# Performance work log

Hardware: AMD Instinct MI355X
Metric: run time of the kernel (lower is better)

The kernel has to match this reference:

```python
import jax, jax.numpy as jnp
import numpy as np

B, CIN, COUT, H, W = 8, 64, 64, 96, 96
K = 3
PAD = 1
BN_EPS = 1e-5


def conv2d(x, w, b):
    # plain 3x3 conv, stride 1, pad 1 (NCHW / OIHW)
    y = jax.lax.conv_general_dilated(
        x, w, window_strides=(1, 1), padding=[(PAD, PAD), (PAD, PAD)],
        dimension_numbers=("NCHW", "OIHW", "NCHW"))
    return y + b[None, :, None, None]


def setup_inputs() -> dict:
    key = jax.random.key(0)
    ks = jax.random.split(key, 6)
    s = 0.05  # small init so offsets stay near the regular grid (matches DCN zero-ish init)
    return {
        "x": jax.random.normal(ks[0], (B, CIN, H, W), jnp.float32),
        "offset_w": jax.random.normal(ks[1], (2 * K * K, CIN, K, K), jnp.float32) * s,
        "offset_b": jnp.zeros((2 * K * K,), jnp.float32),
        "mod_w": jax.random.normal(ks[2], (K * K, CIN, K, K), jnp.float32) * s,
        "mod_b": jnp.zeros((K * K,), jnp.float32),
        "weight": jax.random.normal(ks[3], (COUT, CIN, K, K), jnp.float32) * s,
        "bias": jax.random.normal(ks[4], (COUT,), jnp.float32) * s,
        "bn_gamma": jnp.ones((COUT,), jnp.float32),
        "bn_beta": jnp.zeros((COUT,), jnp.float32),
        "bn_mean": jnp.zeros((COUT,), jnp.float32),
        "bn_var": jnp.ones((COUT,), jnp.float32),
    }


def _deform_sample(xb, py, px):
    # xb: [C,H,W]; py, px: [K2,H,W] fractional sampling coords (zero outside image)
    y0 = jnp.floor(py)
    x0 = jnp.floor(px)
    dy = py - y0
    dx = px - x0

    def gather(yi, xi):
        valid = ((yi >= 0) & (yi < H) & (xi >= 0) & (xi < W)).astype(xb.dtype)
        yc = jnp.clip(yi, 0, H - 1).astype(jnp.int32)
        xc = jnp.clip(xi, 0, W - 1).astype(jnp.int32)
        return xb[:, yc, xc] * valid  # [C,K2,H,W]

    v00 = gather(y0, x0)
    v01 = gather(y0, x0 + 1.0)
    v10 = gather(y0 + 1.0, x0)
    v11 = gather(y0 + 1.0, x0 + 1.0)
    return (v00 * (1 - dy) * (1 - dx) + v01 * (1 - dy) * dx
            + v10 * dy * (1 - dx) + v11 * dy * dx)  # [C,K2,H,W]


def reference(x, offset_w, offset_b, mod_w, mod_b, weight, bias,
              bn_gamma, bn_beta, bn_mean, bn_var):
    # 1) predict offsets and modulation mask (DCNv2)
    offset = conv2d(x, offset_w, offset_b)                 # [B, 2*K2, H, W]
    modulator = 2.0 * jax.nn.sigmoid(conv2d(x, mod_w, mod_b))  # [B, K2, H, W]

    off = offset.reshape(B, K * K, 2, H, W)
    off_y, off_x = off[:, :, 0], off[:, :, 1]              # [B,K2,H,W]

    # 2) base sampling grid per kernel tap
    ky, kx = jnp.meshgrid(jnp.arange(K), jnp.arange(K), indexing="ij")
    base_y = (jnp.arange(H)[None, :, None] - PAD
              + ky.reshape(-1)[:, None, None]).astype(jnp.float32)  # [K2,H,1]
    base_x = (jnp.arange(W)[None, None, :] - PAD
              + kx.reshape(-1)[:, None, None]).astype(jnp.float32)  # [K2,1,W]
    py = base_y + off_y                                    # [B,K2,H,W]
    px = base_x + off_x

    # 3) bilinear gather at irregular positions, modulate per tap
    sampled = jax.vmap(_deform_sample)(x, py, px)          # [B,C,K2,H,W]
    sampled = sampled * modulator[:, None]                 # broadcast over C

    # 4) contract taps with the regular conv weight
    wk = weight.reshape(COUT, CIN, K * K)
    y = jnp.einsum("bckhw,ock->bohw", sampled, wk) + bias[None, :, None, None]

    # 5) BatchNorm (inference: running stats) + ReLU
    inv = bn_gamma / jnp.sqrt(bn_var + BN_EPS)
    y = (y - bn_mean[None, :, None, None]) * inv[None, :, None, None] \
        + bn_beta[None, :, None, None]
    return jax.nn.relu(y)
```

## Files before the change

kernel.cpp:

```cpp
#include <hip/hip_runtime.h>
#include <hip/hip_bf16.h>
#include <hip/hip_fp16.h>
#include <math.h>

#define BB 8
#define HH 96
#define WW 96
#define HW 9216
#define BN_EPS 1e-5f

typedef _Float16 f16x8 __attribute__((ext_vector_type(8)));
typedef float f32x4 __attribute__((ext_vector_type(4)));

union HU { _Float16 h; unsigned short u; };

#define OFF_W4   0
#define SZ_W4    (BB*9*HW*16)
#define OFF_XT   (OFF_W4 + SZ_W4)
#define SZ_XT    (BB*HW*64*2)
#define OFF_XY   (OFF_XT + SZ_XT)
#define SZ_XY    (BB*9*HW*4)
#define OFF_WB   (OFF_XY + SZ_XY)
#define SZ_WB    (64*576*2)
#define OFF_WO   (OFF_WB + SZ_WB)
#define SZ_WO    (32*576*2)
#define OFF_BN   (OFF_WO + SZ_WO)
#define SZ_BN    (64*2*4)

__global__ __launch_bounds__(256) void prep_kernel(
    const float* __restrict__ weight, const float* __restrict__ offw,
    const float* __restrict__ modw,
    const float* __restrict__ bias, const float* __restrict__ gamma,
    const float* __restrict__ beta, const float* __restrict__ mean,
    const float* __restrict__ var,
    _Float16* __restrict__ wB, _Float16* __restrict__ wOff,
    float* __restrict__ bnS, float* __restrict__ bnB) {
  int tid = blockIdx.x * 256 + threadIdx.x;
  if (tid < 64 * 576) {
    int o = tid / 576, ck = tid % 576;
    int k = ck >> 6, c = ck & 63;
    wB[tid] = (_Float16)weight[o * 576 + c * 9 + k];
  }
  int t2 = tid - 64 * 576;
  if (t2 >= 0 && t2 < 32 * 576) {
    int oc = t2 / 576, kcol = t2 % 576;
    int kk = kcol >> 6, c = kcol & 63;
    float v = 0.f;
    if (oc < 18)      v = offw[(oc * 64 + c) * 9 + kk];
    else if (oc < 27) v = modw[((oc - 18) * 64 + c) * 9 + kk];
    wOff[t2] = (_Float16)v;
  }
  int t3 = tid - (64 * 576 + 32 * 576);
  if (t3 >= 0 && t3 < 64) {
    float inv = gamma[t3] * rsqrtf(var[t3] + BN_EPS);
    bnS[t3] = inv;
    bnB[t3] = (bias[t3] - mean[t3]) * inv + beta[t3];
  }
}

__global__ __launch_bounds__(256) void transpose_x_kernel(
    const float* __restrict__ x, _Float16* __restrict__ xT) {
  __shared__ float tile[64][65];
  int tid = threadIdx.x;
  int b = blockIdx.x & 7;
  int hwb = (blockIdx.x >> 3) * 64;
  int col = tid & 63, g = tid >> 6;
  float r[16];
#pragma unroll
  for (int it = 0; it < 16; ++it)
    r[it] = x[(b * 64 + it * 4 + g) * HW + hwb + col];
  __builtin_amdgcn_sched_barrier(0);
#pragma unroll
  for (int it = 0; it < 16; ++it)
    tile[it * 4 + g][col] = r[it];
  __syncthreads();
#pragma unroll
  for (int it = 0; it < 16; ++it) {
    int p = it * 4 + g;
    xT[(size_t)(b * HW + hwb + p) * 64 + col] = (_Float16)tile[col][p];
  }
}

__global__ __launch_bounds__(256, 8) void conv_offsets_kernel(
    const _Float16* __restrict__ xTh, const _Float16* __restrict__ wOff,
    const float* __restrict__ offb, const float* __restrict__ modb,
    float4* __restrict__ w4, unsigned* __restrict__ xy) {
  __shared__ __attribute__((aligned(16))) _Float16 sN[3 * 34 * 70];
  __shared__ float o_off[32 * 33];

  int tid = threadIdx.x;
  int lane = tid & 63;
  int wv = __builtin_amdgcn_readfirstlane(tid >> 6);

  int bi = blockIdx.x;
  int b = bi & 7, rem = bi >> 3;
  int h = rem / 3, w0 = (rem % 3) * 32;

  const _Float16* xb = xTh + (size_t)b * HW * 64;
  _Float16 sv[26];
#pragma unroll
  for (int i = 0; i < 26; ++i) {
    int p = wv + 4 * i;
    _Float16 v = (_Float16)0.f;
    if (p < 102) {
      int row = p / 34, col = p - row * 34;
      int y = h + row - 1, xx = w0 + col - 1;
      if ((y >= 0) && (y < HH) && (xx >= 0) && (xx < WW))
        v = xb[(size_t)(y * WW + xx) * 64 + lane];
    }
    sv[i] = v;
  }
  __builtin_amdgcn_sched_barrier(0);
#pragma unroll
  for (int i = 0; i < 26; ++i) {
    int p = wv + 4 * i;
    if (p < 102) {
      int row = p / 34, col = p - row * 34;
      sN[(row * 34 + col) * 70 + lane] = sv[i];
    }
  }
  __syncthreads();

  int r = lane & 15, g = lane >> 4;
  int mt = wv >> 1, nt = wv & 1;
  int px = mt * 16 + r;
  const _Float16* bp = wOff + (nt * 16 + r) * 576 + g * 8;
  f32x4 acc = {0.f, 0.f, 0.f, 0.f};
#pragma unroll
  for (int s = 0; s < 18; ++s) {
    int kk = s >> 1, ky = kk / 3, kx = kk - ky * 3;
    f16x8 a = *(const f16x8*)&sN[(ky * 34 + px + kx) * 70 + (s & 1) * 32 + g * 8];
    f16x8 bb = *(const f16x8*)(bp + s * 32);
    acc = __builtin_amdgcn_mfma_f32_16x16x32_f16(a, bb, acc, 0, 0, 0);
  }
#pragma unroll
  for (int j = 0; j < 4; ++j)
    o_off[(mt * 16 + g * 4 + j) * 33 + nt * 16 + r] = acc[j];
  __syncthreads();

  for (int it = tid; it < 288; it += 256) {
    int pxx = it & 31, k = it >> 5;
    int ky = k / 3, kx = k - ky * 3;
    int w = w0 + pxx;

    float offy = o_off[pxx * 33 + 2 * k]     + offb[2 * k];
    float offx = o_off[pxx * 33 + 2 * k + 1] + offb[2 * k + 1];
    float mod  = 2.f / (1.f + __expf(-(o_off[pxx * 33 + 18 + k] + modb[k])));

    float py  = (float)(h - 1 + ky) + offy;
    float px_ = (float)(w - 1 + kx) + offx;
    float y0f = floorf(py), x0f = floorf(px_);
    float dy = py - y0f, dx = px_ - x0f;
    int y0 = (int)y0f, x0 = (int)x0f;
    int y1 = y0 + 1, x1 = x0 + 1;
    bool vy0 = (y0 >= 0) && (y0 < HH), vy1 = (y1 >= 0) && (y1 < HH);
    bool vx0 = (x0 >= 0) && (x0 < WW), vx1 = (x1 >= 0) && (x1 < WW);
    float w00 = (vy0 && vx0) ? (1.f - dy) * (1.f - dx) * mod : 0.f;
    float w01 = (vy0 && vx1) ? (1.f - dy) * dx * mod : 0.f;
    float w10 = (vy1 && vx0) ? dy * (1.f - dx) * mod : 0.f;
    float w11 = (vy1 && vx1) ? dy * dx * mod : 0.f;
    int y0c = min(max(y0, 0), HH - 1), y1c = min(max(y1, 0), HH - 1);
    int x0c = min(max(x0, 0), WW - 1), x1c = min(max(x1, 0), WW - 1);
    unsigned pk = (unsigned)y0c | ((unsigned)y1c << 8) |
                  ((unsigned)x0c << 16) | ((unsigned)x1c << 24);
    int idx = (b * 9 + k) * HW + h * WW + w;
    w4[idx] = make_float4(w00, w01, w10, w11);
    xy[idx] = pk;
  }
}

__device__ __forceinline__ float hf(unsigned u) {
  HU h; h.u = (unsigned short)u; return (float)h.h;
}

__global__ __launch_bounds__(256, 4) void dcn_main_kernel(
    const _Float16* __restrict__ xT,
    const float4* __restrict__ w4, const unsigned* __restrict__ xy,
    const _Float16* __restrict__ wB,
    const float* __restrict__ bnS, const float* __restrict__ bnB,
    float* __restrict__ out) {
  __shared__ __attribute__((aligned(16))) _Float16 s_A[16 * 584];
  float* o_lds = (float*)s_A;

  int tid = threadIdx.x;
  int lane = tid & 63;
  int wv = __builtin_amdgcn_readfirstlane(tid >> 6);

  int bi = blockIdx.x;
  int b = bi & 7, t = bi >> 3;
  int h = t / 6, w0 = (t - (t / 6) * 6) * 16;
  int hwrow = h * WW + w0;

  const _Float16* xb = xT + (size_t)b * HW * 64;
  unsigned lane2 = (unsigned)(lane << 1);

  float4 wjA[9], wjB[9];
  unsigned rA[36], rB[36];

#define ISSUE(RES, WJ, P)                                                    \
  {                                                                          \
    int hw = hwrow + wv * 4 + (P);                                           \
    _Pragma("unroll")                                                        \
    for (int k = 0; k < 9; ++k) {                                            \
      int idx = (b * 9 + k) * HW + hw;                                       \
      unsigned q = xy[idx];                                                  \
      WJ[k] = w4[idx];                                                       \
      unsigned y0 = q & 255u, y1 = (q >> 8) & 255u;                          \
      unsigned x0 = (q >> 16) & 255u, x1 = q >> 24;                          \
      unsigned s00 = (y0 * WW + x0) << 7, s01 = (y0 * WW + x1) << 7;         \
      unsigned s10 = (y1 * WW + x0) << 7, s11 = (y1 * WW + x1) << 7;         \
      asm volatile("global_load_ushort %0, %1, %2"                           \
                   : "=v"(RES[4 * k + 0]) : "v"(s00 + lane2), "s"(xb));      \
      asm volatile("global_load_ushort %0, %1, %2"                           \
                   : "=v"(RES[4 * k + 1]) : "v"(s01 + lane2), "s"(xb));      \
      asm volatile("global_load_ushort %0, %1, %2"                           \
                   : "=v"(RES[4 * k + 2]) : "v"(s10 + lane2), "s"(xb));      \
      asm volatile("global_load_ushort %0, %1, %2"                           \
                   : "=v"(RES[4 * k + 3]) : "v"(s11 + lane2), "s"(xb));      \
    }                                                                        \
  }

#define COMBINE(RES, WJ, P)                                                  \
  {                                                                          \
    int pl = wv * 4 + (P);                                                   \
    _Pragma("unroll")                                                        \
    for (int k = 0; k < 9; ++k) {                                            \
      float4 wj = WJ[k];                                                     \
      float s = wj.x * hf(RES[4 * k + 0]) + wj.y * hf(RES[4 * k + 1])        \
              + wj.z * hf(RES[4 * k + 2]) + wj.w * hf(RES[4 * k + 3]);       \
      s_A[pl * 584 + k * 64 + lane] = (_Float16)s;                           \
    }                                                                        \
  }

#define WAITV(N)                                                             \
  asm volatile("s_waitcnt vmcnt(" #N ")" ::: "memory");                      \
  __builtin_amdgcn_sched_barrier(0);

  ISSUE(rA, wjA, 0)
  ISSUE(rB, wjB, 1)
  WAITV(36)
  COMBINE(rA, wjA, 0)
  ISSUE(rA, wjA, 2)
  WAITV(36)
  COMBINE(rB, wjB, 1)
  ISSUE(rB, wjB, 3)
  WAITV(36)
  COMBINE(rA, wjA, 2)
  WAITV(0)
  COMBINE(rB, wjB, 3)

#undef ISSUE
#undef COMBINE
#undef WAITV

  __syncthreads();

  int r = lane & 15, g = lane >> 4;
  const _Float16* arow = s_A + r * 584 + g * 8;
  const _Float16* bp = wB + (wv * 16 + r) * 576 + g * 8;
  f32x4 accA = {0.f, 0.f, 0.f, 0.f}, accB = {0.f, 0.f, 0.f, 0.f};
#pragma unroll 3
  for (int s = 0; s < 18; s += 2) {
    f16x8 a0 = *(const f16x8*)(arow + s * 32);
    f16x8 b0 = *(const f16x8*)(bp + s * 32);
    f16x8 a1 = *(const f16x8*)(arow + s * 32 + 32);
    f16x8 b1 = *(const f16x8*)(bp + s * 32 + 32);
    accA = __builtin_amdgcn_mfma_f32_16x16x32_f16(a0, b0, accA, 0, 0, 0);
    accB = __builtin_amdgcn_mfma_f32_16x16x32_f16(a1, b1, accB, 0, 0, 0);
  }

  int o = wv * 16 + r;
  float sc = bnS[o], sh = bnB[o];
  __syncthreads();
#pragma unroll
  for (int j = 0; j < 4; ++j) {
    int px = g * 4 + j;
    o_lds[o * 20 + px] = fmaxf((accA[j] + accB[j]) * sc + sh, 0.f);
  }
  __syncthreads();

  int oo = tid >> 2, q = tid & 3;
  float4 u = *(const float4*)&o_lds[oo * 20 + q * 4];
  *(float4*)(out + (size_t)(b * 64 + oo) * HW + hwrow + q * 4) = u;
}

extern "C" void kernel_launch(void* const* d_in, const int* in_sizes, int n_in,
                              void* d_out, int out_size, void* d_ws, size_t ws_size,
                              hipStream_t stream) {
  const float* x      = (const float*)d_in[0];
  const float* offw   = (const float*)d_in[1];
  const float* offb   = (const float*)d_in[2];
  const float* modw   = (const float*)d_in[3];
  const float* modb   = (const float*)d_in[4];
  const float* weight = (const float*)d_in[5];
  const float* bias   = (const float*)d_in[6];
  const float* gamma  = (const float*)d_in[7];
  const float* beta   = (const float*)d_in[8];
  const float* mean   = (const float*)d_in[9];
  const float* var    = (const float*)d_in[10];

  char* ws = (char*)d_ws;
  float4*    w4    = (float4*)(ws + OFF_W4);
  _Float16*  xTh   = (_Float16*)(ws + OFF_XT);
  unsigned*  xybuf = (unsigned*)(ws + OFF_XY);
  _Float16*  wB    = (_Float16*)(ws + OFF_WB);
  _Float16*  wOff  = (_Float16*)(ws + OFF_WO);
  float*     bnS   = (float*)(ws + OFF_BN);
  float*     bnB   = bnS + 64;

  prep_kernel<<<217, 256, 0, stream>>>(weight, offw, modw, bias, gamma, beta,
                                       mean, var, wB, wOff, bnS, bnB);
  transpose_x_kernel<<<1152, 256, 0, stream>>>(x, xTh);
  conv_offsets_kernel<<<2304, 256, 0, stream>>>(xTh, wOff, offb, modb, w4, xybuf);
  dcn_main_kernel<<<4608, 256, 0, stream>>>(xTh, w4, xybuf, wB, bnS, bnB,
                                            (float*)d_out);
}
```

Before: 106.8 us.

## Stage bilinear gather corners via global_load_lds 16-byte transfers into an LDS ring

The per-lane 2-byte global_load_ushort gathers of the four bilinear corners are replaced by 16-byte global-to-LDS DMA loads. Each wave now issues 18 vector loads instead of 144, feeding a four-slot LDS staging ring with a software-pipelined issue/wait/combine schedule. Precomputed corner offsets are shared through a small LDS table, and the bilinear weights are loaded inside the combine step. The aim is to cut gather instruction count and improve memory coalescing. The costs are extra LDS footprint and a fragile vmcnt accounting, since the w4 loads inside the combine step may force extra waits.

```diff
diff --git a/kernel.cpp b/kernel.cpp
--- a/kernel.cpp
+++ b/kernel.cpp
@@ -13,6 +13,9 @@
 typedef float f32x4 __attribute__((ext_vector_type(4)));
 
 union HU { _Float16 h; unsigned short u; };
+
+typedef const __attribute__((address_space(1))) unsigned char g1_t;
+typedef __attribute__((address_space(3))) unsigned char l3_t;
 
 #define OFF_W4   0
 #define SZ_W4    (BB*9*HW*16)
@@ -169,8 +172,8 @@
   }
 }
 
-__device__ __forceinline__ float hf(unsigned u) {
-  HU h; h.u = (unsigned short)u; return (float)h.h;
+__device__ __forceinline__ float hf(unsigned short u) {
+  HU h; h.u = u; return (float)h.h;
 }
 
 __global__ __launch_bounds__(256, 4) void dcn_main_kernel(
@@ -180,6 +183,8 @@
     const float* __restrict__ bnS, const float* __restrict__ bnB,
     float* __restrict__ out) {
   __shared__ __attribute__((aligned(16))) _Float16 s_A[16 * 584];
+  __shared__ __attribute__((aligned(16))) unsigned char stage[4][4][1024];
+  __shared__ unsigned offs[4][144];
   float* o_lds = (float*)s_A;
 
   int tid = threadIdx.x;
@@ -192,66 +197,97 @@
   int hwrow = h * WW + w0;
 
   const _Float16* xb = xT + (size_t)b * HW * 64;
-  unsigned lane2 = (unsigned)(lane << 1);
-
-  float4 wjA[9], wjB[9];
-  unsigned rA[36], rB[36];
-
-#define ISSUE(RES, WJ, P)                                                    \
-  {                                                                          \
-    int hw = hwrow + wv * 4 + (P);                                           \
-    _Pragma("unroll")                                                        \
-    for (int k = 0; k < 9; ++k) {                                            \
-      int idx = (b * 9 + k) * HW + hw;                                       \
-      unsigned q = xy[idx];                                                  \
-      WJ[k] = w4[idx];                                                       \
-      unsigned y0 = q & 255u, y1 = (q >> 8) & 255u;                          \
-      unsigned x0 = (q >> 16) & 255u, x1 = q >> 24;                          \
-      unsigned s00 = (y0 * WW + x0) << 7, s01 = (y0 * WW + x1) << 7;         \
-      unsigned s10 = (y1 * WW + x0) << 7, s11 = (y1 * WW + x1) << 7;         \
-      asm volatile("global_load_ushort %0, %1, %2"                           \
-                   : "=v"(RES[4 * k + 0]) : "v"(s00 + lane2), "s"(xb));      \
-      asm volatile("global_load_ushort %0, %1, %2"                           \
-                   : "=v"(RES[4 * k + 1]) : "v"(s01 + lane2), "s"(xb));      \
-      asm volatile("global_load_ushort %0, %1, %2"                           \
-                   : "=v"(RES[4 * k + 2]) : "v"(s10 + lane2), "s"(xb));      \
-      asm volatile("global_load_ushort %0, %1, %2"                           \
-                   : "=v"(RES[4 * k + 3]) : "v"(s11 + lane2), "s"(xb));      \
-    }                                                                        \
-  }
-
-#define COMBINE(RES, WJ, P)                                                  \
-  {                                                                          \
-    int pl = wv * 4 + (P);                                                   \
-    _Pragma("unroll")                                                        \
-    for (int k = 0; k < 9; ++k) {                                            \
-      float4 wj = WJ[k];                                                     \
-      float s = wj.x * hf(RES[4 * k + 0]) + wj.y * hf(RES[4 * k + 1])        \
-              + wj.z * hf(RES[4 * k + 2]) + wj.w * hf(RES[4 * k + 3]);       \
-      s_A[pl * 584 + k * 64 + lane] = (_Float16)s;                           \
-    }                                                                        \
-  }
+  const unsigned char* xbc = (const unsigned char*)xb;
+
+  if (lane < 36) {
+    int px = lane / 9, k = lane - px * 9;
+    unsigned q = xy[(b * 9 + k) * HW + hwrow + wv * 4 + px];
+    unsigned y0 = q & 255u, y1 = (q >> 8) & 255u;
+    unsigned x0 = (q >> 16) & 255u, x1 = q >> 24;
+    unsigned o00 = (y0 * WW + x0) << 7, o01 = (y0 * WW + x1) << 7;
+    unsigned o10 = (y1 * WW + x0) << 7, o11 = (y1 * WW + x1) << 7;
+    *(uint4*)&offs[wv][lane * 4] = make_uint4(o00, o01, o10, o11);
+  }
+
+  unsigned adr[18];
+#pragma unroll
+  for (int i = 0; i < 18; ++i) {
+    int tidx;
+    if (i < 16) tidx = ((i >> 2) * 9 + (i & 3) * 2 + (lane >> 5)) * 4 + ((lane >> 3) & 3);
+    else        tidx = (((i - 16) * 2 + (lane >> 5)) * 9 + 8) * 4 + ((lane >> 3) & 3);
+    adr[i] = offs[wv][tidx] + (unsigned)((lane & 7) << 4);
+  }
+
+#define ISSUE(I)                                                             \
+  __builtin_amdgcn_global_load_lds((g1_t*)(xbc + adr[I]),                    \
+                                   (l3_t*)&stage[wv][(I) & 3][0], 16, 0, 0);
 
 #define WAITV(N)                                                             \
   asm volatile("s_waitcnt vmcnt(" #N ")" ::: "memory");                      \
   __builtin_amdgcn_sched_barrier(0);
 
-  ISSUE(rA, wjA, 0)
-  ISSUE(rB, wjB, 1)
-  WAITV(36)
-  COMBINE(rA, wjA, 0)
-  ISSUE(rA, wjA, 2)
-  WAITV(36)
-  COMBINE(rB, wjB, 1)
-  ISSUE(rB, wjB, 3)
-  WAITV(36)
-  COMBINE(rA, wjA, 2)
-  WAITV(0)
-  COMBINE(rB, wjB, 3)
+#define COMBA(I)                                                             \
+  {                                                                          \
+    const int px_ = (I) >> 2, k0_ = ((I) & 3) * 2, pl_ = wv * 4 + px_;       \
+    const unsigned char* st_ = &stage[wv][(I) & 3][0];                       \
+    _Pragma("unroll")                                                        \
+    for (int dk = 0; dk < 2; ++dk) {                                         \
+      int k_ = k0_ + dk;                                                     \
+      float4 wj = w4[(b * 9 + k_) * HW + hwrow + pl_];                       \
+      const unsigned char* p_ = st_ + dk * 512 + (lane << 1);                \
+      unsigned short u0 = *(const unsigned short*)(p_ + 0);                  \
+      unsigned short u1 = *(const unsigned short*)(p_ + 128);                \
+      unsigned short u2 = *(const unsigned short*)(p_ + 256);                \
+      unsigned short u3 = *(const unsigned short*)(p_ + 384);                \
+      float s = wj.x * hf(u0) + wj.y * hf(u1) + wj.z * hf(u2) + wj.w * hf(u3); \
+      s_A[pl_ * 584 + k_ * 64 + lane] = (_Float16)s;                         \
+    }                                                                        \
+  }                                                                          \
+  __builtin_amdgcn_sched_barrier(0);
+
+#define COMBB(I)                                                             \
+  {                                                                          \
+    const int pxb_ = ((I) - 16) * 2;                                         \
+    const unsigned char* st_ = &stage[wv][(I) & 3][0];                       \
+    _Pragma("unroll")                                                        \
+    for (int po = 0; po < 2; ++po) {                                         \
+      int pl_ = wv * 4 + pxb_ + po;                                          \
+      float4 wj = w4[(b * 9 + 8) * HW + hwrow + pl_];                        \
+      const unsigned char* p_ = st_ + po * 512 + (lane << 1);                \
+      unsigned short u0 = *(const unsigned short*)(p_ + 0);                  \
+      unsigned short u1 = *(const unsigned short*)(p_ + 128);                \
+      unsigned short u2 = *(const unsigned short*)(p_ + 256);                \
+      unsigned short u3 = *(const unsigned short*)(p_ + 384);                \
+      float s = wj.x * hf(u0) + wj.y * hf(u1) + wj.z * hf(u2) + wj.w * hf(u3); \
+      s_A[pl_ * 584 + 8 * 64 + lane] = (_Float16)s;                          \
+    }                                                                        \
+  }                                                                          \
+  __builtin_amdgcn_sched_barrier(0);
+
+  ISSUE(0) ISSUE(1) ISSUE(2)
+  WAITV(2) COMBA(0)  ISSUE(3)
+  WAITV(2) COMBA(1)  ISSUE(4)
+  WAITV(2) COMBA(2)  ISSUE(5)
+  WAITV(2) COMBA(3)  ISSUE(6)
+  WAITV(2) COMBA(4)  ISSUE(7)
+  WAITV(2) COMBA(5)  ISSUE(8)
+  WAITV(2) COMBA(6)  ISSUE(9)
+  WAITV(2) COMBA(7)  ISSUE(10)
+  WAITV(2) COMBA(8)  ISSUE(11)
+  WAITV(2) COMBA(9)  ISSUE(12)
+  WAITV(2) COMBA(10) ISSUE(13)
+  WAITV(2) COMBA(11) ISSUE(14)
+  WAITV(2) COMBA(12) ISSUE(15)
+  WAITV(2) COMBA(13) ISSUE(16)
+  WAITV(2) COMBA(14) ISSUE(17)
+  WAITV(2) COMBA(15)
+  WAITV(1) COMBB(16)
+  WAITV(0) COMBB(17)
 
 #undef ISSUE
-#undef COMBINE
 #undef WAITV
+#undef COMBA
+#undef COMBB
 
   __syncthreads();
 
```

After: 116.6 us. +9.2%, slower.
